# Optimization experiments

Hardware: AMD Instinct MI355X
Metric: run time of the kernel (lower is better)

The kernel has to match this reference:

```python
import jax, jax.numpy as jnp
import numpy as np

S, B, C = 7, 2, 20
LAMBDA_COORD = 5.0
LAMBDA_NOOBJ = 0.5
WH_EPS = 1e-6
IOU_EPS = 1e-6
BATCH = 16384


def _iou_yolo(a, b):
    # a, b: [..., 4] in (cx, cy, w, h) 'yolo' center format
    ax1, ay1 = a[..., 0] - a[..., 2] / 2, a[..., 1] - a[..., 3] / 2
    ax2, ay2 = a[..., 0] + a[..., 2] / 2, a[..., 1] + a[..., 3] / 2
    bx1, by1 = b[..., 0] - b[..., 2] / 2, b[..., 1] - b[..., 3] / 2
    bx2, by2 = b[..., 0] + b[..., 2] / 2, b[..., 1] + b[..., 3] / 2
    iw = jnp.clip(jnp.minimum(ax2, bx2) - jnp.maximum(ax1, bx1), 0.0)
    ih = jnp.clip(jnp.minimum(ay2, by2) - jnp.maximum(ay1, by1), 0.0)
    inter = iw * ih
    area_a = jnp.abs((ax2 - ax1) * (ay2 - ay1))
    area_b = jnp.abs((bx2 - bx1) * (by2 - by1))
    return inter / (area_a + area_b - inter + IOU_EPS)


def setup_inputs() -> dict:
    key = jax.random.key(0)
    k1, k2, k3 = jax.random.split(key, 3)
    D = C + 5 * B  # 30
    y_trues = jax.random.uniform(k1, (BATCH, S, S, D), dtype=jnp.float32)
    # conf channel must be exactly 0.0 or 1.0 (loss branches on == 1)
    conf = (jax.random.uniform(k2, (BATCH, S, S)) < 0.3).astype(jnp.float32)
    y_trues = y_trues.at[..., 4].set(conf)
    y_preds = jax.random.normal(k3, (BATCH, S, S, D), dtype=jnp.float32)
    return {"y_trues": y_trues, "y_preds": y_preds}


def reference(y_trues, y_preds):
    D = C + 5 * B
    t = y_trues.reshape(-1, S * S, D)   # [N, 49, 30]
    p = y_preds.reshape(-1, S * S, D)
    batch_size = p.shape[0]

    b = t[..., 0:4]
    bhat1 = p[..., 0:4]
    bhat2 = p[..., 5:9]

    iou1 = _iou_yolo(b, bhat1)          # [N, 49]
    iou2 = _iou_yolo(b, bhat2)
    use1 = iou1 > iou2

    bhat = jnp.where(use1[..., None], bhat1, bhat2)            # responsible box
    confhat_chosen = jnp.where(use1, p[..., 4], p[..., 9])
    confhat_other = jnp.where(use1, p[..., 9], p[..., 4])

    # coord losses (object cells)
    xy = LAMBDA_COORD * ((b[..., 0] - bhat[..., 0]) ** 2 + (b[..., 1] - bhat[..., 1]) ** 2)
    wh = LAMBDA_COORD * (
        (jnp.sqrt(b[..., 2]) - jnp.sqrt(jnp.abs(bhat[..., 2] + WH_EPS))) ** 2
        + (jnp.sqrt(b[..., 3]) - jnp.sqrt(jnp.abs(bhat[..., 3] + WH_EPS))) ** 2
    )
    obj_conf = (t[..., 4] - confhat_chosen) ** 2
    noobj_in_obj = LAMBDA_NOOBJ * (0.0 - confhat_other) ** 2
    cls = jnp.sum((t[..., 10:] - p[..., 10:]) ** 2, axis=-1)

    obj_terms = xy + wh + obj_conf + noobj_in_obj + cls

    # no-object cells: penalize both predicted confs toward y_true conf (== target conf channel)
    noobj_terms = LAMBDA_NOOBJ * (
        (t[..., 4] - p[..., 4]) ** 2 + (t[..., 4] - p[..., 9]) ** 2
    )

    obj_mask = t[..., 4] == 1.0
    total = jnp.sum(jnp.where(obj_mask, obj_terms, noobj_terms))
    return total / batch_size
```

## Files before the change

### kernel.cpp

```cpp
#include <hip/hip_runtime.h>

#define LAMBDA_COORD 5.0f
#define LAMBDA_NOOBJ 0.5f
#define WH_EPS 1e-6f
#define IOU_EPS 1e-6f

constexpr int BLOCKS = 1792;

__device__ __forceinline__ float iou_yolo(float a0, float a1, float a2, float a3,
                                          float b0, float b1, float b2, float b3) {
    float ax1 = a0 - a2 * 0.5f, ay1 = a1 - a3 * 0.5f;
    float ax2 = a0 + a2 * 0.5f, ay2 = a1 + a3 * 0.5f;
    float bx1 = b0 - b2 * 0.5f, by1 = b1 - b3 * 0.5f;
    float bx2 = b0 + b2 * 0.5f, by2 = b1 + b3 * 0.5f;
    float iw = fmaxf(fminf(ax2, bx2) - fmaxf(ax1, bx1), 0.0f);
    float ih = fmaxf(fminf(ay2, by2) - fmaxf(ay1, by1), 0.0f);
    float inter = iw * ih;
    float area_a = fabsf((ax2 - ax1) * (ay2 - ay1));
    float area_b = fabsf((bx2 - bx1) * (by2 - by1));
    return inter / (area_a + area_b - inter + IOU_EPS);
}

__device__ __forceinline__ float cell_terms(
    float b0, float b1, float b2, float b3, float t4,
    float p0, float p1, float p2, float p3, float p4,
    float p5, float p6, float p7, float p8, float p9) {
    float iou1 = iou_yolo(b0, b1, b2, b3, p0, p1, p2, p3);
    float iou2 = iou_yolo(b0, b1, b2, b3, p5, p6, p7, p8);
    bool use1 = iou1 > iou2;

    float bh0 = use1 ? p0 : p5;
    float bh1 = use1 ? p1 : p6;
    float bh2 = use1 ? p2 : p7;
    float bh3 = use1 ? p3 : p8;
    float conf_c = use1 ? p4 : p9;
    float conf_o = use1 ? p9 : p4;

    float dx = b0 - bh0, dy = b1 - bh1;
    float xy = LAMBDA_COORD * (dx * dx + dy * dy);

    float sw = sqrtf(b2) - sqrtf(fabsf(bh2 + WH_EPS));
    float sh = sqrtf(b3) - sqrtf(fabsf(bh3 + WH_EPS));
    float wh = LAMBDA_COORD * (sw * sw + sh * sh);

    float dc = t4 - conf_c;
    float obj_terms = xy + wh + dc * dc + LAMBDA_NOOBJ * conf_o * conf_o;

    float d4 = t4 - p4, d9 = t4 - p9;
    float noobj_terms = LAMBDA_NOOBJ * (d4 * d4 + d9 * d9);

    return (t4 == 1.0f) ? obj_terms : noobj_terms;
}

__global__ __launch_bounds__(256) void yolo_loss_kernel(
    const float4* __restrict__ tv, const float4* __restrict__ pv,
    float* __restrict__ out, int ngroups, float inv_batch) {
    const int lane = threadIdx.x & 63;
    const int widx = threadIdx.x >> 6;
    const int wave_id = blockIdx.x * 4 + widx;
    const int nwaves = gridDim.x * 4;

    const int u = lane % 15;
    const int bbase = lane - u;
    const bool active = lane < 60;

    float cm[4];
#pragma unroll
    for (int j = 0; j < 4; ++j) {
        int idx = 4 * u + j;
        bool isA = (idx >= 10 && idx < 30);
        bool isB = (idx >= 40);
        cm[j] = (isA || isB) ? 1.0f : 0.0f;
    }
    const bool sideA = (u <= 7);

    float v = 0.0f;

    for (int g = wave_id; g < ngroups; g += nwaves) {
        float4 T = make_float4(0.f, 0.f, 0.f, 0.f);
        float4 P = make_float4(0.f, 0.f, 0.f, 0.f);
        if (active) {
            size_t base = (size_t)g * 60 + lane;
            T = tv[base];
            P = pv[base];
        }

        float d0 = T.x - P.x, d1 = T.y - P.y, d2 = T.z - P.z, d3 = T.w - P.w;
        float s_cls = d0 * d0 * cm[0] + d1 * d1 * cm[1] +
                      d2 * d2 * cm[2] + d3 * d3 * cm[3];

        float t4A = __shfl(T.x, bbase + 1, 64);
        float t4B = __shfl(T.z, bbase + 8, 64);
        float objm = ((sideA ? t4A : t4B) == 1.0f) ? 1.0f : 0.0f;
        v += s_cls * objm;

        float a_b0 = __shfl(T.x, bbase, 64);
        float a_b1 = __shfl(T.y, bbase, 64);
        float a_b2 = __shfl(T.z, bbase, 64);
        float a_b3 = __shfl(T.w, bbase, 64);
        float a_p0 = __shfl(P.x, bbase, 64);
        float a_p1 = __shfl(P.y, bbase, 64);
        float a_p2 = __shfl(P.z, bbase, 64);
        float a_p3 = __shfl(P.w, bbase, 64);
        float a_p8 = __shfl(P.x, bbase + 2, 64);
        float a_p9 = __shfl(P.y, bbase + 2, 64);

        float b_b0 = __shfl(T.z, bbase + 7, 64);
        float b_b1 = __shfl(T.w, bbase + 7, 64);
        float b_p0 = __shfl(P.z, bbase + 7, 64);
        float b_p1 = __shfl(P.w, bbase + 7, 64);
        float b_p6 = __shfl(P.x, bbase + 9, 64);
        float b_p7 = __shfl(P.y, bbase + 9, 64);
        float b_p8 = __shfl(P.z, bbase + 9, 64);
        float b_p9 = __shfl(P.w, bbase + 9, 64);

        float cA = cell_terms(a_b0, a_b1, a_b2, a_b3, T.x,
                              a_p0, a_p1, a_p2, a_p3, P.x,
                              P.y, P.z, P.w, a_p8, a_p9);
        float cB = cell_terms(b_b0, b_b1, T.x, T.y, T.z,
                              b_p0, b_p1, P.x, P.y, P.z,
                              P.w, b_p6, b_p7, b_p8, b_p9);
        if (active && u == 1) v += cA;
        if (active && u == 8) v += cB;
    }

#pragma unroll
    for (int off = 32; off > 0; off >>= 1)
        v += __shfl_down(v, off, 64);

    __shared__ float swave[4];
    if ((threadIdx.x & 63) == 0) swave[widx] = v;
    __syncthreads();
    if (threadIdx.x == 0) {
        float s = swave[0] + swave[1] + swave[2] + swave[3];
        atomicAdd(out, s * inv_batch);
    }
}

extern "C" void kernel_launch(void* const* d_in, const int* in_sizes, int n_in,
                              void* d_out, int out_size, void* d_ws, size_t ws_size,
                              hipStream_t stream) {
    const float* t = (const float*)d_in[0];
    const float* p = (const float*)d_in[1];
    float* out = (float*)d_out;

    const int total = in_sizes[0];
    const int cells = total / 30;
    const int ngroups = cells / 8;
    const int batch = cells / 49;
    const float inv_batch = 1.0f / (float)batch;

    hipMemsetAsync(out, 0, sizeof(float), stream);

    yolo_loss_kernel<<<BLOCKS, 256, 0, stream>>>(
        (const float4*)t, (const float4*)p, out, ngroups, inv_batch);
}
```

Measured before the change: 212.9 us.

## Compute per-cell box terms on 8 lanes with direct loads instead of shuffles

Drops the 18 cross-lane shuffles that broadcast box and confidence fields to every lane, each of which then evaluated two full cell loss computations. Lanes 0-7 now each re-read their cell's first ten fields from global memory (mostly cache hits) and compute the IoU/coord/object terms once. The no-object confidence terms are split across lanes 1, 2, 8 and 9. This trades shuffle and ALU work for extra small redundant loads; the kernel is likely memory-bound, so the gain depends on how much the ALU/shuffle work was exposed.

Measured after the change: 209.3 us. No clear change (-1.7%).

```diff
diff --git a/kernel.cpp b/kernel.cpp
--- a/kernel.cpp
+++ b/kernel.cpp
@@ -7,72 +7,28 @@
 
 constexpr int BLOCKS = 1792;
 
-__device__ __forceinline__ float iou_yolo(float a0, float a1, float a2, float a3,
-                                          float b0, float b1, float b2, float b3) {
-    float ax1 = a0 - a2 * 0.5f, ay1 = a1 - a3 * 0.5f;
-    float ax2 = a0 + a2 * 0.5f, ay2 = a1 + a3 * 0.5f;
-    float bx1 = b0 - b2 * 0.5f, by1 = b1 - b3 * 0.5f;
-    float bx2 = b0 + b2 * 0.5f, by2 = b1 + b3 * 0.5f;
-    float iw = fmaxf(fminf(ax2, bx2) - fmaxf(ax1, bx1), 0.0f);
-    float ih = fmaxf(fminf(ay2, by2) - fmaxf(ay1, by1), 0.0f);
-    float inter = iw * ih;
-    float area_a = fabsf((ax2 - ax1) * (ay2 - ay1));
-    float area_b = fabsf((bx2 - bx1) * (by2 - by1));
-    return inter / (area_a + area_b - inter + IOU_EPS);
-}
-
-__device__ __forceinline__ float cell_terms(
-    float b0, float b1, float b2, float b3, float t4,
-    float p0, float p1, float p2, float p3, float p4,
-    float p5, float p6, float p7, float p8, float p9) {
-    float iou1 = iou_yolo(b0, b1, b2, b3, p0, p1, p2, p3);
-    float iou2 = iou_yolo(b0, b1, b2, b3, p5, p6, p7, p8);
-    bool use1 = iou1 > iou2;
-
-    float bh0 = use1 ? p0 : p5;
-    float bh1 = use1 ? p1 : p6;
-    float bh2 = use1 ? p2 : p7;
-    float bh3 = use1 ? p3 : p8;
-    float conf_c = use1 ? p4 : p9;
-    float conf_o = use1 ? p9 : p4;
-
-    float dx = b0 - bh0, dy = b1 - bh1;
-    float xy = LAMBDA_COORD * (dx * dx + dy * dy);
-
-    float sw = sqrtf(b2) - sqrtf(fabsf(bh2 + WH_EPS));
-    float sh = sqrtf(b3) - sqrtf(fabsf(bh3 + WH_EPS));
-    float wh = LAMBDA_COORD * (sw * sw + sh * sh);
-
-    float dc = t4 - conf_c;
-    float obj_terms = xy + wh + dc * dc + LAMBDA_NOOBJ * conf_o * conf_o;
-
-    float d4 = t4 - p4, d9 = t4 - p9;
-    float noobj_terms = LAMBDA_NOOBJ * (d4 * d4 + d9 * d9);
-
-    return (t4 == 1.0f) ? obj_terms : noobj_terms;
-}
-
 __global__ __launch_bounds__(256) void yolo_loss_kernel(
-    const float4* __restrict__ tv, const float4* __restrict__ pv,
+    const float* __restrict__ t_g, const float* __restrict__ p_g,
     float* __restrict__ out, int ngroups, float inv_batch) {
     const int lane = threadIdx.x & 63;
     const int widx = threadIdx.x >> 6;
     const int wave_id = blockIdx.x * 4 + widx;
-    const int nwaves = gridDim.x * 4;
+    const int nwaves = BLOCKS * 4;
 
     const int u = lane % 15;
     const int bbase = lane - u;
     const bool active = lane < 60;
+    const bool sideA = (u <= 7);
 
     float cm[4];
 #pragma unroll
     for (int j = 0; j < 4; ++j) {
         int idx = 4 * u + j;
-        bool isA = (idx >= 10 && idx < 30);
-        bool isB = (idx >= 40);
-        cm[j] = (isA || isB) ? 1.0f : 0.0f;
+        cm[j] = ((idx >= 10 && idx < 30) || idx >= 40) ? 1.0f : 0.0f;
     }
-    const bool sideA = (u <= 7);
+
+    const float4* tv = (const float4*)t_g;
+    const float4* pv = (const float4*)p_g;
 
     float v = 0.0f;
 
@@ -80,9 +36,24 @@
         float4 T = make_float4(0.f, 0.f, 0.f, 0.f);
         float4 P = make_float4(0.f, 0.f, 0.f, 0.f);
         if (active) {
-            size_t base = (size_t)g * 60 + lane;
-            T = tv[base];
-            P = pv[base];
+            size_t b = (size_t)g * 60 + lane;
+            T = tv[b];
+            P = pv[b];
+        }
+
+        float2 a01 = {0.f, 0.f}, a23 = {0.f, 0.f};
+        float2 q01 = {0.f, 0.f}, q23 = {0.f, 0.f}, q45 = {0.f, 0.f},
+               q67 = {0.f, 0.f}, q89 = {0.f, 0.f};
+        float tt4 = 0.f;
+        if (lane < 8) {
+            const size_t cb = ((size_t)g * 8 + lane) * 30;
+            const float2* tc = (const float2*)(t_g + cb);
+            const float2* pc = (const float2*)(p_g + cb);
+            a01 = tc[0]; a23 = tc[1];
+            tt4 = t_g[cb + 4];
+            q01 = pc[0]; q23 = pc[1];
+            q45 = pc[2]; q67 = pc[3];
+            q89 = pc[4];
         }
 
         float d0 = T.x - P.x, d1 = T.y - P.y, d2 = T.z - P.z, d3 = T.w - P.w;
@@ -91,37 +62,59 @@
 
         float t4A = __shfl(T.x, bbase + 1, 64);
         float t4B = __shfl(T.z, bbase + 8, 64);
-        float objm = ((sideA ? t4A : t4B) == 1.0f) ? 1.0f : 0.0f;
+        float t4s = sideA ? t4A : t4B;
+        float objm = (t4s == 1.0f) ? 1.0f : 0.0f;
         v += s_cls * objm;
 
-        float a_b0 = __shfl(T.x, bbase, 64);
-        float a_b1 = __shfl(T.y, bbase, 64);
-        float a_b2 = __shfl(T.z, bbase, 64);
-        float a_b3 = __shfl(T.w, bbase, 64);
-        float a_p0 = __shfl(P.x, bbase, 64);
-        float a_p1 = __shfl(P.y, bbase, 64);
-        float a_p2 = __shfl(P.z, bbase, 64);
-        float a_p3 = __shfl(P.w, bbase, 64);
-        float a_p8 = __shfl(P.x, bbase + 2, 64);
-        float a_p9 = __shfl(P.y, bbase + 2, 64);
+        float nb = 0.f;
+        if (u == 1)      { float d = t4A - P.x; nb = d * d; }
+        else if (u == 2) { float d = t4A - P.y; nb = d * d; }
+        else if (u == 8) { float d = t4B - P.z; nb = d * d; }
+        else if (u == 9) { float d = t4B - P.w; nb = d * d; }
+        if (active) v += LAMBDA_NOOBJ * nb * (1.0f - objm);
 
-        float b_b0 = __shfl(T.z, bbase + 7, 64);
-        float b_b1 = __shfl(T.w, bbase + 7, 64);
-        float b_p0 = __shfl(P.z, bbase + 7, 64);
-        float b_p1 = __shfl(P.w, bbase + 7, 64);
-        float b_p6 = __shfl(P.x, bbase + 9, 64);
-        float b_p7 = __shfl(P.y, bbase + 9, 64);
-        float b_p8 = __shfl(P.z, bbase + 9, 64);
-        float b_p9 = __shfl(P.w, bbase + 9, 64);
+        {
+            float ax1 = a01.x - a23.x * 0.5f, ay1 = a01.y - a23.y * 0.5f;
+            float ax2 = a01.x + a23.x * 0.5f, ay2 = a01.y + a23.y * 0.5f;
+            float area_a = fabsf((ax2 - ax1) * (ay2 - ay1));
 
-        float cA = cell_terms(a_b0, a_b1, a_b2, a_b3, T.x,
-                              a_p0, a_p1, a_p2, a_p3, P.x,
-                              P.y, P.z, P.w, a_p8, a_p9);
-        float cB = cell_terms(b_b0, b_b1, T.x, T.y, T.z,
-                              b_p0, b_p1, P.x, P.y, P.z,
-                              P.w, b_p6, b_p7, b_p8, b_p9);
-        if (active && u == 1) v += cA;
-        if (active && u == 8) v += cB;
+            float b1x1 = q01.x - q23.x * 0.5f, b1y1 = q01.y - q23.y * 0.5f;
+            float b1x2 = q01.x + q23.x * 0.5f, b1y2 = q01.y + q23.y * 0.5f;
+            float b2x1 = q45.y - q67.y * 0.5f, b2y1 = q67.x - q89.x * 0.5f;
+            float b2x2 = q45.y + q67.y * 0.5f, b2y2 = q67.x + q89.x * 0.5f;
+
+            float iw1 = fmaxf(fminf(ax2, b1x2) - fmaxf(ax1, b1x1), 0.0f);
+            float ih1 = fmaxf(fminf(ay2, b1y2) - fmaxf(ay1, b1y1), 0.0f);
+            float in1 = iw1 * ih1;
+            float ar1 = fabsf((b1x2 - b1x1) * (b1y2 - b1y1));
+            float iou1 = in1 / (area_a + ar1 - in1 + IOU_EPS);
+
+            float iw2 = fmaxf(fminf(ax2, b2x2) - fmaxf(ax1, b2x1), 0.0f);
+            float ih2 = fmaxf(fminf(ay2, b2y2) - fmaxf(ay1, b2y1), 0.0f);
+            float in2 = iw2 * ih2;
+            float ar2 = fabsf((b2x2 - b2x1) * (b2y2 - b2y1));
+            float iou2 = in2 / (area_a + ar2 - in2 + IOU_EPS);
+
+            bool use1 = iou1 > iou2;
+            float bh0 = use1 ? q01.x : q45.y;
+            float bh1 = use1 ? q01.y : q67.x;
+            float bh2 = use1 ? q23.x : q67.y;
+            float bh3 = use1 ? q23.y : q89.x;
+            float cc  = use1 ? q45.x : q89.y;
+            float co  = use1 ? q89.y : q45.x;
+
+            float dx = a01.x - bh0, dy = a01.y - bh1;
+            float xy = LAMBDA_COORD * (dx * dx + dy * dy);
+
+            float sw = sqrtf(a23.x) - sqrtf(fabsf(bh2 + WH_EPS));
+            float sh = sqrtf(a23.y) - sqrtf(fabsf(bh3 + WH_EPS));
+            float wh = LAMBDA_COORD * (sw * sw + sh * sh);
+
+            float dc = tt4 - cc;
+            float obj_part = xy + wh + dc * dc + LAMBDA_NOOBJ * co * co;
+
+            if (lane < 8 && tt4 == 1.0f) v += obj_part;
+        }
     }
 
 #pragma unroll
@@ -152,6 +145,5 @@
 
     hipMemsetAsync(out, 0, sizeof(float), stream);
 
-    yolo_loss_kernel<<<BLOCKS, 256, 0, stream>>>(
-        (const float4*)t, (const float4*)p, out, ngroups, inv_batch);
+    yolo_loss_kernel<<<BLOCKS, 256, 0, stream>>>(t, p, out, ngroups, inv_batch);
 }
```
